# Optimization experiments

Hardware: AMD Instinct MI355X
Metric: run time of the kernel (lower is better)

## Reference

```python
import jax, jax.numpy as jnp
import numpy as np

IN_CH, IN_U, OUT_CH, OUT_U = 1152, 8, 10, 16
BATCH = 256
ROUTING_EPOCH = 3


def squash(s, axis=-1):
    # v = (||s||^2 / (1 + ||s||^2)) * s / ||s||
    sqn = jnp.sum(s * s, axis=axis, keepdims=True)
    return s * (sqn / ((1.0 + sqn) * jnp.sqrt(sqn + 1e-9)))


def setup_inputs() -> dict:
    key = jax.random.key(0)
    k1, k2 = jax.random.split(key)
    inp = jax.random.normal(k1, (BATCH, IN_CH, IN_U), dtype=jnp.float32)
    W = jax.random.normal(k2, (IN_CH, OUT_CH, OUT_U, IN_U), dtype=jnp.float32)
    return {"inp": inp, "W": W}


def reference(inp, W):
    # u_hat[b,i,o,u] = sum_k W[i,o,u,k] * inp[b,i,k]   -> [B, 1152, 10, 16]
    u_hat = jnp.einsum('iouk,bik->biou', W, inp)
    B = inp.shape[0]
    b = jnp.zeros((IN_CH, OUT_CH), dtype=inp.dtype)  # routing logits [1152, 10]
    v = None
    for _ in range(ROUTING_EPOCH):
        c = jax.nn.softmax(b, axis=1)                 # [1152, 10]
        s = jnp.einsum('biou,io->bou', u_hat, c)      # sum over input capsules -> [B, 10, 16]
        v = squash(s, axis=-1)                        # [B, 10, 16]
        # delta_b[i,o] = mean_b sum_u u_hat[b,i,o,u] * v[b,o,u]
        b = b + jnp.einsum('biou,bou->io', u_hat, v) / B
    return v  # == original v.squeeze(): [B, 10, 16]
```

## Files before the change

### kernel.cpp

```cpp
#include <hip/hip_runtime.h>
#include <math.h>

#define NB 256
#define IC 1152
#define OC 10
#define OU 16
#define IK 8
#define KTOT (IC * IK)
#define NTOT (OC * OU)
#define S_KS 16

typedef __attribute__((ext_vector_type(8))) short short8;
typedef __attribute__((ext_vector_type(4))) float f32x4;

static __device__ __forceinline__ unsigned short f2bf(float f) {
    unsigned u = __float_as_uint(f);
    unsigned r = (u + 0x7FFF + ((u >> 16) & 1)) >> 16;
    return (unsigned short)r;
}

__global__ __launch_bounds__(256) void prep_kernel(
    const float* __restrict__ inp,
    float* __restrict__ blog,
    unsigned short* __restrict__ inpb,
    unsigned short* __restrict__ inpT)
{
    const int kt  = blockIdx.x;
    const int bt  = blockIdx.y;
    const int tid = threadIdx.x;

    {
        int bid = blockIdx.y * 144 + blockIdx.x;
        if (bid < 45) blog[bid * 256 + tid] = 0.f;
    }

    __shared__ unsigned short sh[64][65];

#pragma unroll
    for (int j = 0; j < 4; ++j) {
        int q     = j * 256 + tid;
        int b_loc = q >> 4;
        int kq    = (q & 15) * 4;
        float4 g = *(const float4*)&inp[(size_t)(bt * 64 + b_loc) * KTOT + kt * 64 + kq];
        unsigned short h0 = f2bf(g.x), h1 = f2bf(g.y), h2 = f2bf(g.z), h3 = f2bf(g.w);
        sh[kq][b_loc] = h0; sh[kq + 1][b_loc] = h1;
        sh[kq + 2][b_loc] = h2; sh[kq + 3][b_loc] = h3;
        short4 pk = { (short)h0, (short)h1, (short)h2, (short)h3 };
        *(short4*)&inpb[(size_t)(bt * 64 + b_loc) * KTOT + kt * 64 + kq] = pk;
    }
    __syncthreads();

#pragma unroll
    for (int j = 0; j < 4; ++j) {
        int q     = j * 256 + tid;
        int k_loc = q >> 4;
        int b4    = (q & 15) * 4;
        short4 pk = { (short)sh[k_loc][b4],     (short)sh[k_loc][b4 + 1],
                      (short)sh[k_loc][b4 + 2], (short)sh[k_loc][b4 + 3] };
        *(short4*)&inpT[(size_t)(kt * 64 + k_loc) * 256 + bt * 64 + b4] = pk;
    }
}

__global__ __launch_bounds__(256) void wc_kernel(
    const float* __restrict__ W,
    const float* __restrict__ blog,
    unsigned short* __restrict__ wct)
{
    const int i = blockIdx.x, tid = threadIdx.x;
    __shared__ float c_sh[OC];
    if (tid < OC) {
        const float* br = &blog[(size_t)i * OC];
        float x[OC], m = -1e30f;
#pragma unroll
        for (int o = 0; o < OC; ++o) { x[o] = br[o]; m = fmaxf(m, x[o]); }
        float ssum = 0.f;
#pragma unroll
        for (int o = 0; o < OC; ++o) ssum += expf(x[o] - m);
        c_sh[tid] = expf(x[tid] - m) / ssum;
    }
    __syncthreads();
    if (tid < NTOT) {
        const float cc = c_sh[tid >> 4];
        const float* wr = &W[(size_t)i * 1280 + tid * 8];
        float4 a = *(const float4*)wr;
        float4 b = *(const float4*)(wr + 4);
        union { short8 v; unsigned short u[8]; } pk;
        pk.u[0] = f2bf(cc * a.x); pk.u[1] = f2bf(cc * a.y);
        pk.u[2] = f2bf(cc * a.z); pk.u[3] = f2bf(cc * a.w);
        pk.u[4] = f2bf(cc * b.x); pk.u[5] = f2bf(cc * b.y);
        pk.u[6] = f2bf(cc * b.z); pk.u[7] = f2bf(cc * b.w);
        *(short8*)&wct[(size_t)tid * KTOT + (size_t)i * 8] = pk.v;
    }
}

__global__ __launch_bounds__(256) void spass_kernel(
    const unsigned short* __restrict__ inpb,
    const unsigned short* __restrict__ wct,
    float* __restrict__ part)
{
    const int g    = blockIdx.x * 4 + (threadIdx.x >> 6);
    const int lane = threadIdx.x & 63;
    const int ks   = g & 15;
    const int mt   = (g >> 4) & 15;
    const int nt   = g >> 8;
    const int l15  = lane & 15;
    const int koff = (lane >> 4) * 8;
    const int k0   = ks * 576;

    const unsigned short* ap = inpb + (size_t)(mt * 16 + l15) * KTOT + k0 + koff;
    const unsigned short* bp = wct  + (size_t)(nt * 16 + l15) * KTOT + k0 + koff;

    f32x4 acc = {0.f, 0.f, 0.f, 0.f};
#pragma unroll
    for (int kk = 0; kk < 18; ++kk) {
        short8 av = *(const short8*)(ap + kk * 32);
        short8 bv = *(const short8*)(bp + kk * 32);
        acc = __builtin_amdgcn_mfma_f32_16x16x32_bf16(av, bv, acc, 0, 0, 0);
    }

    float* pp = part + ((size_t)ks * NB + mt * 16 + (lane >> 4) * 4) * NTOT + nt * 16 + l15;
#pragma unroll
    for (int r = 0; r < 4; ++r)
        pp[(size_t)r * NTOT] = acc[r];
}

__global__ __launch_bounds__(256) void reduce_squash_kernel(
    const float* __restrict__ part, float* __restrict__ vout,
    unsigned short* __restrict__ vT)
{
    const int tid = threadIdx.x;
    const int el  = tid & 31;
    const int kl  = tid >> 5;
    const int e   = blockIdx.x * 32 + el;

    float a = part[(size_t)(kl * 2) * (NB * NTOT) + e]
            + part[(size_t)(kl * 2 + 1) * (NB * NTOT) + e];

    __shared__ float red[8][36];
    red[kl][el] = a;
    __syncthreads();

    if (tid < 32) {
        float s = ((red[0][el] + red[1][el]) + (red[2][el] + red[3][el]))
                + ((red[4][el] + red[5][el]) + (red[6][el] + red[7][el]));
        float sq = s * s;
        sq += __shfl_xor(sq, 1);
        sq += __shfl_xor(sq, 2);
        sq += __shfl_xor(sq, 4);
        sq += __shfl_xor(sq, 8);
        float vv = s * (sq / ((1.f + sq) * sqrtf(sq + 1e-9f)));
        vout[e] = vv;
        int n = e % NTOT, b = e / NTOT;
        vT[(size_t)n * 256 + b] = f2bf(vv);
    }
}

__global__ __launch_bounds__(256) void delta_kernel(
    const unsigned short* __restrict__ inpT,
    const unsigned short* __restrict__ vT,
    const float* __restrict__ W,
    float* __restrict__ blog)
{
    const int g    = blockIdx.x * 4 + (threadIdx.x >> 6);
    const int lane = threadIdx.x & 63;
    const int mt   = g % 576;
    const int nt   = g / 576;
    const int l15  = lane & 15;
    const int quad = lane >> 4;
    const int koff = quad * 8;

    const unsigned short* ap = inpT + (size_t)(mt * 16 + l15) * 256 + koff;
    const unsigned short* bp = vT   + (size_t)(nt * 16 + l15) * 256 + koff;

    f32x4 acc = {0.f, 0.f, 0.f, 0.f};
#pragma unroll
    for (int kk = 0; kk < 8; ++kk) {
        short8 av = *(const short8*)(ap + kk * 32);
        short8 bv = *(const short8*)(bp + kk * 32);
        acc = __builtin_amdgcn_mfma_f32_16x16x32_bf16(av, bv, acc, 0, 0, 0);
    }

    const int i = mt * 2 + (quad >> 1);
    const float* wr = W + (((size_t)i * OC + nt) * OU + l15) * IK + (quad & 1) * 4;
    float4 wf = *(const float4*)wr;
    float wsum = wf.x * acc[0] + wf.y * acc[1] + wf.z * acc[2] + wf.w * acc[3];

    wsum += __shfl_xor(wsum, 16);
    wsum += __shfl_xor(wsum, 1);
    wsum += __shfl_xor(wsum, 2);
    wsum += __shfl_xor(wsum, 4);
    wsum += __shfl_xor(wsum, 8);

    if ((lane & 31) == 0)
        blog[(size_t)i * OC + nt] += wsum * (1.0f / NB);
}

extern "C" void kernel_launch(void* const* d_in, const int* in_sizes, int n_in,
                              void* d_out, int out_size, void* d_ws, size_t ws_size,
                              hipStream_t stream) {
    const float* inp = (const float*)d_in[0];
    const float* W   = (const float*)d_in[1];
    float* vout = (float*)d_out;

    float* blog = (float*)d_ws;
    float* part = blog + IC * OC;
    unsigned short* inpb = (unsigned short*)(part + (size_t)S_KS * NB * NTOT);
    unsigned short* wct  = inpb + (size_t)NB * KTOT;
    unsigned short* inpT = wct + (size_t)NTOT * KTOT;
    unsigned short* vT   = inpT + (size_t)KTOT * 256;

    prep_kernel<<<dim3(144, 4), dim3(256), 0, stream>>>(inp, blog, inpb, inpT);

    for (int t = 0; t < 3; ++t) {
        wc_kernel<<<dim3(IC), dim3(256), 0, stream>>>(W, blog, wct);
        spass_kernel<<<dim3(640), dim3(256), 0, stream>>>(inpb, wct, part);
        reduce_squash_kernel<<<dim3(NB * NTOT / 32), dim3(256), 0, stream>>>(part, vout, vT);
        if (t < 2)
            delta_kernel<<<dim3(1440), dim3(256), 0, stream>>>(inpT, vT, W, blog);
    }
}
```

Before: 158.3 us.

## Fuse softmax-weighted W conversion into spass kernel via LDS staging

```diff
diff --git a/kernel.cpp b/kernel.cpp
--- a/kernel.cpp
+++ b/kernel.cpp
@@ -61,60 +61,68 @@
     }
 }
 
-__global__ __launch_bounds__(256) void wc_kernel(
+#define BLP 584
+__global__ __launch_bounds__(256) void spass_kernel(
+    const unsigned short* __restrict__ inpb,
     const float* __restrict__ W,
     const float* __restrict__ blog,
-    unsigned short* __restrict__ wct)
-{
-    const int i = blockIdx.x, tid = threadIdx.x;
-    __shared__ float c_sh[OC];
-    if (tid < OC) {
-        const float* br = &blog[(size_t)i * OC];
-        float x[OC], m = -1e30f;
-#pragma unroll
-        for (int o = 0; o < OC; ++o) { x[o] = br[o]; m = fmaxf(m, x[o]); }
-        float ssum = 0.f;
-#pragma unroll
-        for (int o = 0; o < OC; ++o) ssum += expf(x[o] - m);
-        c_sh[tid] = expf(x[tid] - m) / ssum;
-    }
-    __syncthreads();
-    if (tid < NTOT) {
-        const float cc = c_sh[tid >> 4];
-        const float* wr = &W[(size_t)i * 1280 + tid * 8];
-        float4 a = *(const float4*)wr;
-        float4 b = *(const float4*)(wr + 4);
-        union { short8 v; unsigned short u[8]; } pk;
-        pk.u[0] = f2bf(cc * a.x); pk.u[1] = f2bf(cc * a.y);
-        pk.u[2] = f2bf(cc * a.z); pk.u[3] = f2bf(cc * a.w);
-        pk.u[4] = f2bf(cc * b.x); pk.u[5] = f2bf(cc * b.y);
-        pk.u[6] = f2bf(cc * b.z); pk.u[7] = f2bf(cc * b.w);
-        *(short8*)&wct[(size_t)tid * KTOT + (size_t)i * 8] = pk.v;
-    }
-}
-
-__global__ __launch_bounds__(256) void spass_kernel(
-    const unsigned short* __restrict__ inpb,
-    const unsigned short* __restrict__ wct,
     float* __restrict__ part)
 {
-    const int g    = blockIdx.x * 4 + (threadIdx.x >> 6);
-    const int lane = threadIdx.x & 63;
-    const int ks   = g & 15;
-    const int mt   = (g >> 4) & 15;
-    const int nt   = g >> 8;
+    const int bid  = blockIdx.x;
+    const int nt   = bid % 10;
+    const int ks   = (bid / 10) % 16;
+    const int mtg  = bid / 160;
+    const int tid  = threadIdx.x;
+    const int w    = tid >> 6;
+    const int lane = tid & 63;
     const int l15  = lane & 15;
     const int koff = (lane >> 4) * 8;
     const int k0   = ks * 576;
-
-    const unsigned short* ap = inpb + (size_t)(mt * 16 + l15) * KTOT + k0 + koff;
-    const unsigned short* bp = wct  + (size_t)(nt * 16 + l15) * KTOT + k0 + koff;
+    const int i0   = ks * 72;
+    const int mt   = mtg * 4 + w;
+
+    __shared__ unsigned short Bl[16 * BLP];
+    __shared__ float c_loc[72];
+
+    if (tid < 72) {
+        const float* br = &blog[(size_t)(i0 + tid) * OC];
+        float x[OC], m = -1e30f;
+#pragma unroll
+        for (int o = 0; o < OC; ++o) { x[o] = br[o]; m = fmaxf(m, x[o]); }
+        float ssum = 0.f;
+#pragma unroll
+        for (int o = 0; o < OC; ++o) ssum += expf(x[o] - m);
+        c_loc[tid] = expf(x[nt] - m) / ssum;
+    }
+    __syncthreads();
+
+#pragma unroll
+    for (int jj = 0; jj < 5; ++jj) {
+        int q = jj * 256 + tid;
+        if (q < 1152) {
+            int i_loc = q >> 4, u = q & 15;
+            const float* wr = W + (((size_t)(i0 + i_loc) * OC + nt) * OU + u) * IK;
+            float4 a = *(const float4*)wr;
+            float4 b = *(const float4*)(wr + 4);
+            float cc = c_loc[i_loc];
+            union { short8 v; unsigned short us[8]; } pk;
+            pk.us[0] = f2bf(cc * a.x); pk.us[1] = f2bf(cc * a.y);
+            pk.us[2] = f2bf(cc * a.z); pk.us[3] = f2bf(cc * a.w);
+            pk.us[4] = f2bf(cc * b.x); pk.us[5] = f2bf(cc * b.y);
+            pk.us[6] = f2bf(cc * b.z); pk.us[7] = f2bf(cc * b.w);
+            *(short8*)&Bl[u * BLP + i_loc * 8] = pk.v;
+        }
+    }
+    __syncthreads();
+
+    const unsigned short* ap  = inpb + (size_t)(mt * 16 + l15) * KTOT + k0 + koff;
+    const unsigned short* bls = &Bl[l15 * BLP + koff];
 
     f32x4 acc = {0.f, 0.f, 0.f, 0.f};
 #pragma unroll
     for (int kk = 0; kk < 18; ++kk) {
         short8 av = *(const short8*)(ap + kk * 32);
-        short8 bv = *(const short8*)(bp + kk * 32);
+        short8 bv = *(const short8*)(bls + kk * 32);
         acc = __builtin_amdgcn_mfma_f32_16x16x32_bf16(av, bv, acc, 0, 0, 0);
     }
 
@@ -205,15 +213,13 @@
     float* blog = (float*)d_ws;
     float* part = blog + IC * OC;
     unsigned short* inpb = (unsigned short*)(part + (size_t)S_KS * NB * NTOT);
-    unsigned short* wct  = inpb + (size_t)NB * KTOT;
-    unsigned short* inpT = wct + (size_t)NTOT * KTOT;
+    unsigned short* inpT = inpb + (size_t)NB * KTOT;
     unsigned short* vT   = inpT + (size_t)KTOT * 256;
 
     prep_kernel<<<dim3(144, 4), dim3(256), 0, stream>>>(inp, blog, inpb, inpT);
 
     for (int t = 0; t < 3; ++t) {
-        wc_kernel<<<dim3(IC), dim3(256), 0, stream>>>(W, blog, wct);
-        spass_kernel<<<dim3(640), dim3(256), 0, stream>>>(inpb, wct, part);
+        spass_kernel<<<dim3(640), dim3(256), 0, stream>>>(inpb, W, blog, part);
         reduce_squash_kernel<<<dim3(NB * NTOT / 32), dim3(256), 0, stream>>>(part, vout, vT);
         if (t < 2)
             delta_kernel<<<dim3(1440), dim3(256), 0, stream>>>(inpT, vT, W, blog);
```

Measured after the change: 132.8 us. 1.19x faster.
